# Performance work log

Hardware: AMD Instinct MI355X
Metric: run time of the kernel (lower is better)

The kernel has to match this reference:

```python
import jax, jax.numpy as jnp
import numpy as np

N, E = 50000, 800000
IN_DIM, HID, ZDIM = 256, 128, 64
LN_EPS = 1e-5


def _layernorm(x, gamma, beta):
    mu = jnp.mean(x, axis=-1, keepdims=True)
    var = jnp.mean(jnp.square(x - mu), axis=-1, keepdims=True)
    return (x - mu) * jax.lax.rsqrt(var + LN_EPS) * gamma + beta


def _gcn_conv(h, src, dst, dinv, W, b):
    # h: (N, d_in) -> (N, d_out). GCNConv: X W, then sym-normalized
    # aggregation over edges with self-loops, then bias.
    h = h @ W                                   # (N, d_out)
    coef = dinv[src] * dinv[dst]                # (E,)
    agg = jax.ops.segment_sum(h[src] * coef[:, None], dst,
                              num_segments=h.shape[0])
    agg = agg + h * jnp.square(dinv)[:, None]   # self-loop term
    return agg + b


def setup_inputs() -> dict:
    key = jax.random.key(0)
    ks = jax.random.split(key, 5)
    x = jax.random.normal(ks[0], (N, IN_DIM), dtype=jnp.float32)
    edge_index = jax.random.randint(ks[1], (2, E), 0, N, dtype=jnp.int64)
    s1 = 1.0 / np.sqrt(IN_DIM)
    s2 = 1.0 / np.sqrt(HID)
    return {
        "x": x,
        "edge_index": edge_index,
        "ln_gamma": jnp.ones((IN_DIM,), jnp.float32),
        "ln_beta": jnp.zeros((IN_DIM,), jnp.float32),
        "W1": jax.random.normal(ks[2], (IN_DIM, HID), jnp.float32) * s1,
        "b1": jnp.zeros((HID,), jnp.float32),
        "W2": jax.random.normal(ks[3], (HID, HID), jnp.float32) * s2,
        "b2": jnp.zeros((HID,), jnp.float32),
        "W3": jax.random.normal(ks[4], (HID, ZDIM), jnp.float32) * s2,
        "b3": jnp.zeros((ZDIM,), jnp.float32),
    }


def reference(x, edge_index, ln_gamma, ln_beta, W1, b1, W2, b2, W3, b3):
    src, dst = edge_index[0], edge_index[1]
    n = x.shape[0]
    # degree with self-loops (dropout is inference no-op, training=False)
    deg = jnp.ones((n,), x.dtype).at[dst].add(1.0)
    dinv = jax.lax.rsqrt(deg)
    h = _layernorm(x, ln_gamma, ln_beta)
    h = jax.nn.relu(_gcn_conv(h, src, dst, dinv, W1, b1))
    h = jax.nn.relu(_gcn_conv(h, src, dst, dinv, W2, b2))
    z = _gcn_conv(h, src, dst, dinv, W3, b3)
    return z
```

## Files before the change

### kernel.cpp

```cpp
#include <hip/hip_runtime.h>
#include <cstdint>
#include <cstddef>


typedef __attribute__((ext_vector_type(8))) __bf16 bf16x8;
typedef __attribute__((ext_vector_type(4))) float f32x4;
typedef _Float16 half_t;
typedef __attribute__((ext_vector_type(8))) _Float16 half8_t;

#define NHIST 256
#define CHUNK 4096
#define MAXB 8192

__global__ __launch_bounds__(256) void prep_misc(
    const int* __restrict__ dst,
    const float* __restrict__ W1, const float* __restrict__ W2,
    const float* __restrict__ W3,
    int* __restrict__ bcnt_multi,
    unsigned short* __restrict__ W1t_hi, unsigned short* __restrict__ W1t_lo,
    unsigned short* __restrict__ W2t_hi, unsigned short* __restrict__ W2t_lo,
    unsigned short* __restrict__ W3t_hi, unsigned short* __restrict__ W3t_lo,
    int E) {
  int blk = blockIdx.x;
  int tid = threadIdx.x;
  if (blk < NHIST) {
    __shared__ int h[256];
    h[tid] = 0;
    __syncthreads();
    for (int e = blk * 256 + tid; e < E; e += NHIST * 256)
      atomicAdd(&h[dst[e] >> 8], 1);
    __syncthreads();
    bcnt_multi[blk * 256 + tid] = h[tid];
    return;
  }
  int idx = (blk - NHIST) * 256 + tid;
  if (idx < 32768) {
    int k = idx / 128, c = idx % 128;
    float v = W1[idx];
    __bf16 h = (__bf16)v;
    __bf16 l = (__bf16)(v - (float)h);
    W1t_hi[(size_t)c * 256 + k] = __builtin_bit_cast(unsigned short, h);
    W1t_lo[(size_t)c * 256 + k] = __builtin_bit_cast(unsigned short, l);
    return;
  }
  const float* W;
  unsigned short *Th, *Tl;
  int K, NOUT;
  if (idx < 49152) {
    idx -= 32768;
    W = W2; Th = W2t_hi; Tl = W2t_lo; K = 128; NOUT = 128;
  } else {
    idx -= 49152;
    W = W3; Th = W3t_hi; Tl = W3t_lo; K = 128; NOUT = 64;
  }
  int k = idx / NOUT, c = idx % NOUT;
  float v = W[idx];
  half_t h = (half_t)v;
  half_t l = (half_t)((v - (float)h) * 2048.0f);
  Th[(size_t)c * K + k] = __builtin_bit_cast(unsigned short, h);
  Tl[(size_t)c * K + k] = __builtin_bit_cast(unsigned short, l);
}

__global__ __launch_bounds__(256) void scan_buckets(const int* __restrict__ bcnt_multi,
                                                    int* __restrict__ bbase,
                                                    int* __restrict__ bcur, int NB, int E) {
  __shared__ int tmp[256];
  int t = threadIdx.x;
  int v = 0;
  for (int h = 0; h < NHIST; ++h) v += bcnt_multi[h * 256 + t];
  tmp[t] = v;
  __syncthreads();
  for (int off = 1; off < 256; off <<= 1) {
    int x = (t >= off) ? tmp[t - off] : 0;
    __syncthreads();
    tmp[t] += x;
    __syncthreads();
  }
  int excl = tmp[t] - v;
  if (t < NB) { bbase[t] = excl; bcur[t] = excl; }
  if (t == 0) bbase[NB] = E;
}

__device__ __forceinline__ void scatter_body(char* smem_raw, int bid,
                                             const int* __restrict__ src,
                                             const int* __restrict__ dst,
                                             int* __restrict__ bcur,
                                             unsigned int* __restrict__ binned, int E) {
  unsigned int* recs = (unsigned int*)smem_raw;
  int* hist = (int*)(smem_raw + 16384);
  int* lbase = hist + 256;
  int* resv = lbase + 256;
  int* cur = resv + 256;
  int t = threadIdx.x;
  int e0 = bid * CHUNK;
  if (e0 >= E) return;
  int len = min(CHUNK, E - e0);
  hist[t] = 0;
  cur[t] = 0;
  __syncthreads();
  for (int i = t; i < len; i += 256) atomicAdd(&hist[dst[e0 + i] >> 8], 1);
  __syncthreads();
  int v = hist[t];
  lbase[t] = v;
  __syncthreads();
  for (int off = 1; off < 256; off <<= 1) {
    int x = (t >= off) ? lbase[t - off] : 0;
    __syncthreads();
    lbase[t] += x;
    __syncthreads();
  }
  int myexcl = lbase[t] - v;
  if (v) resv[t] = atomicAdd(&bcur[t], v);
  __syncthreads();
  lbase[t] = myexcl;
  __syncthreads();
  for (int i = t; i < len; i += 256) {
    int d = dst[e0 + i], s = src[e0 + i];
    int b = d >> 8;
    int r = atomicAdd(&cur[b], 1);
    recs[lbase[b] + r] = ((unsigned int)d << 16) | (unsigned int)s;
  }
  __syncthreads();
  for (int i = t; i < len; i += 256) {
    unsigned int rc = recs[i];
    int b = rc >> 24;
    binned[resv[b] + (i - lbase[b])] = rc;
  }
}

__device__ __forceinline__ void sort_body(char* smem_raw, int b,
                                          const unsigned int* __restrict__ binned,
                                          const int* __restrict__ bbase,
                                          int* __restrict__ srcs,
                                          int* __restrict__ offs,
                                          float* __restrict__ dinv,
                                          int N, int NB, int E) {
  int* sstage = (int*)smem_raw;
  int* hist = (int*)(smem_raw + 32768);
  int* nbase = hist + 256;
  int* cur = nbase + 256;
  int* tmp = cur + 256;
  int t = threadIdx.x;
  int base = bbase[b], end = bbase[b + 1];
  int L = end - base;
  if (L > MAXB) L = MAXB;
  hist[t] = 0;
  __syncthreads();
  for (int i = t; i < L; i += 256)
    atomicAdd(&hist[(binned[base + i] >> 16) & 255], 1);
  __syncthreads();
  int v = hist[t];
  tmp[t] = v;
  __syncthreads();
  for (int off = 1; off < 256; off <<= 1) {
    int x = (t >= off) ? tmp[t - off] : 0;
    __syncthreads();
    tmp[t] += x;
    __syncthreads();
  }
  int excl = tmp[t] - v;
  nbase[t] = excl;
  cur[t] = excl;
  int node = (b << 8) + t;
  if (node < N) {
    offs[node] = base + excl;
    dinv[node] = rsqrtf(1.0f + (float)v);
  }
  if (b == NB - 1 && t == 0) offs[N] = E;
  __syncthreads();
  for (int i = t; i < L; i += 256) {
    unsigned int p = binned[base + i];
    int ld = (p >> 16) & 255;
    int slot = atomicAdd(&cur[ld], 1);
    sstage[slot] = (int)(p & 0xFFFFu);
  }
  __syncthreads();
  for (int i = t; i < L; i += 256) srcs[base + i] = sstage[i];
}

template <int K, int NOUT, bool LN, bool A_FP16>
__device__ __forceinline__ void gemm_body(char* smem_raw, int gbid,
                                          const void* __restrict__ Avoid,
                                          const unsigned short* __restrict__ Wt_hi,
                                          const unsigned short* __restrict__ Wt_lo,
                                          const float* __restrict__ gamma,
                                          const float* __restrict__ beta,
                                          half_t* __restrict__ out, int nrows) {
  constexpr int BM = 32, BK = 32, BKP = BK + 8;
  constexpr int NTW = NOUT / 32;

  const int tid = threadIdx.x;
  const int lane = tid & 63;
  const int w = tid >> 6;
  const int quad = lane >> 4;
  const int l16 = lane & 15;
  const int rg = (w & 1) * 16;
  const int cg = (w >> 1) * (NOUT / 2);
  const int row0 = gbid * BM;

  if constexpr (!A_FP16) {
    unsigned short* As_hi = (unsigned short*)smem_raw;
    unsigned short* As_lo = As_hi + BM * BKP;
    unsigned short* Bs_hi = As_lo + BM * BKP;
    unsigned short* Bs_lo = Bs_hi + NOUT * BKP;
    float* mu_s = (float*)(Bs_lo + NOUT * BKP);
    float* rs_s = mu_s + BM;
    const float* A = (const float*)Avoid;

    if constexpr (LN) {
      int r = tid >> 3;
      int part = tid & 7;
      int grow = row0 + r;
      if (grow > nrows - 1) grow = nrows - 1;
      const float4* rp = (const float4*)(A + (size_t)grow * K);
      float s = 0.f, s2 = 0.f;
#pragma unroll
      for (int j = 0; j < K / 32; ++j) {
        float4 v = rp[part * (K / 32) + j];
        s += v.x + v.y + v.z + v.w;
        s2 += v.x * v.x + v.y * v.y + v.z * v.z + v.w * v.w;
      }
      s += __shfl_xor(s, 1);
      s += __shfl_xor(s, 2);
      s += __shfl_xor(s, 4);
      s2 += __shfl_xor(s2, 1);
      s2 += __shfl_xor(s2, 2);
      s2 += __shfl_xor(s2, 4);
      if (part == 0) {
        float m = s * (1.0f / (float)K);
        float var = s2 * (1.0f / (float)K) - m * m;
        mu_s[r] = m;
        rs_s[r] = rsqrtf(var + 1e-5f);
      }
      __syncthreads();
    }

    f32x4 acc[NTW];
#pragma unroll
    for (int t = 0; t < NTW; ++t) acc[t] = (f32x4){0.f, 0.f, 0.f, 0.f};

    for (int k0 = 0; k0 < K; k0 += BK) {
      {
        int r = tid >> 3;
        int c4 = (tid & 7) * 4;
        int grow = row0 + r;
        if (grow > nrows - 1) grow = nrows - 1;
        float4 v = *(const float4*)&A[(size_t)grow * K + k0 + c4];
        if constexpr (LN) {
          float m = mu_s[r], s = rs_s[r];
          float4 g = *(const float4*)&gamma[k0 + c4];
          float4 b = *(const float4*)&beta[k0 + c4];
          v.x = (v.x - m) * s * g.x + b.x;
          v.y = (v.y - m) * s * g.y + b.y;
          v.z = (v.z - m) * s * g.z + b.z;
          v.w = (v.w - m) * s * g.w + b.w;
        }
        float vv[4] = {v.x, v.y, v.z, v.w};
#pragma unroll
        for (int j = 0; j < 4; ++j) {
          __bf16 h = (__bf16)vv[j];
          __bf16 l = (__bf16)(vv[j] - (float)h);
          As_hi[r * BKP + c4 + j] = __builtin_bit_cast(unsigned short, h);
          As_lo[r * BKP + c4 + j] = __builtin_bit_cast(unsigned short, l);
        }
      }
#pragma unroll
      for (int i = 0; i < NOUT / 64; ++i) {
        int n = i * 64 + (tid >> 2);
        int c8 = (tid & 3) * 8;
        *(uint4*)&Bs_hi[n * BKP + c8] = *(const uint4*)&Wt_hi[(size_t)n * K + k0 + c8];
        *(uint4*)&Bs_lo[n * BKP + c8] = *(const uint4*)&Wt_lo[(size_t)n * K + k0 + c8];
      }
      __syncthreads();

      bf16x8 ah = *(const bf16x8*)&As_hi[(rg + l16) * BKP + quad * 8];
      bf16x8 al = *(const bf16x8*)&As_lo[(rg + l16) * BKP + quad * 8];
#pragma unroll
      for (int t = 0; t < NTW; ++t) {
        bf16x8 bh = *(const bf16x8*)&Bs_hi[(cg + t * 16 + l16) * BKP + quad * 8];
        bf16x8 bl = *(const bf16x8*)&Bs_lo[(cg + t * 16 + l16) * BKP + quad * 8];
        acc[t] = __builtin_amdgcn_mfma_f32_16x16x32_bf16(ah, bh, acc[t], 0, 0, 0);
        acc[t] = __builtin_amdgcn_mfma_f32_16x16x32_bf16(al, bh, acc[t], 0, 0, 0);
        acc[t] = __builtin_amdgcn_mfma_f32_16x16x32_bf16(ah, bl, acc[t], 0, 0, 0);
      }
      __syncthreads();
    }

#pragma unroll
    for (int t = 0; t < NTW; ++t) {
#pragma unroll
      for (int r = 0; r < 4; ++r) {
        int grow = row0 + rg + quad * 4 + r;
        if (grow < nrows)
          out[(size_t)grow * NOUT + cg + t * 16 + l16] = (half_t)acc[t][r];
      }
    }
  } else {
    half_t* As = (half_t*)smem_raw;
    half_t* Bs_hi = As + BM * BKP;
    half_t* Bs_lo = Bs_hi + NOUT * BKP;
    const half_t* A = (const half_t*)Avoid;

    f32x4 acc1[NTW], acc2[NTW];
#pragma unroll
    for (int t = 0; t < NTW; ++t) {
      acc1[t] = (f32x4){0.f, 0.f, 0.f, 0.f};
      acc2[t] = (f32x4){0.f, 0.f, 0.f, 0.f};
    }

    for (int k0 = 0; k0 < K; k0 += BK) {
      {
        int r = tid >> 3;
        int c4 = (tid & 7) * 4;
        int grow = row0 + r;
        if (grow > nrows - 1) grow = nrows - 1;
        *(uint2*)&As[r * BKP + c4] = *(const uint2*)&A[(size_t)grow * K + k0 + c4];
      }
#pragma unroll
      for (int i = 0; i < NOUT / 64; ++i) {
        int n = i * 64 + (tid >> 2);
        int c8 = (tid & 3) * 8;
        *(uint4*)&Bs_hi[n * BKP + c8] =
            *(const uint4*)&Wt_hi[(size_t)n * K + k0 + c8];
        *(uint4*)&Bs_lo[n * BKP + c8] =
            *(const uint4*)&Wt_lo[(size_t)n * K + k0 + c8];
      }
      __syncthreads();

      half8_t av = *(const half8_t*)&As[(rg + l16) * BKP + quad * 8];
#pragma unroll
      for (int t = 0; t < NTW; ++t) {
        half8_t bh = *(const half8_t*)&Bs_hi[(cg + t * 16 + l16) * BKP + quad * 8];
        half8_t bl = *(const half8_t*)&Bs_lo[(cg + t * 16 + l16) * BKP + quad * 8];
        acc1[t] = __builtin_amdgcn_mfma_f32_16x16x32_f16(av, bh, acc1[t], 0, 0, 0);
        acc2[t] = __builtin_amdgcn_mfma_f32_16x16x32_f16(av, bl, acc2[t], 0, 0, 0);
      }
      __syncthreads();
    }

#pragma unroll
    for (int t = 0; t < NTW; ++t) {
#pragma unroll
      for (int r = 0; r < 4; ++r) {
        int grow = row0 + rg + quad * 4 + r;
        if (grow < nrows)
          out[(size_t)grow * NOUT + cg + t * 16 + l16] =
              (half_t)(acc1[t][r] + acc2[t][r] * (1.0f / 2048.0f));
      }
    }
  }
}

constexpr int GEMM1_SMEM = 32 * 40 * 4 + 128 * 40 * 4 + 256;
__global__ __launch_bounds__(256) void fused_scatter_gemm1(
    const int* __restrict__ src, const int* __restrict__ dst,
    int* __restrict__ bcur, unsigned int* __restrict__ binned, int E,
    const float* __restrict__ x,
    const unsigned short* __restrict__ W1t_hi, const unsigned short* __restrict__ W1t_lo,
    const float* __restrict__ gamma, const float* __restrict__ beta,
    half_t* __restrict__ t, int nrows, int nscat) {
  __shared__ __align__(16) char smem[GEMM1_SMEM];
  if ((int)blockIdx.x < nscat)
    scatter_body(smem, blockIdx.x, src, dst, bcur, binned, E);
  else
    gemm_body<256, 128, true, false>(smem, blockIdx.x - nscat, x, W1t_hi, W1t_lo,
                                     gamma, beta, t, nrows);
}

__global__ __launch_bounds__(256) void fused_sort_gemm1(
    const unsigned int* __restrict__ binned, const int* __restrict__ bbase,
    int* __restrict__ srcs, int* __restrict__ offs, float* __restrict__ dinv,
    int N, int NB, int E,
    const float* __restrict__ x,
    const unsigned short* __restrict__ W1t_hi, const unsigned short* __restrict__ W1t_lo,
    const float* __restrict__ gamma, const float* __restrict__ beta,
    half_t* __restrict__ t, int nrows, int g1a) {
  __shared__ __align__(16) char smem[36864];
  if ((int)blockIdx.x < NB)
    sort_body(smem, blockIdx.x, binned, bbase, srcs, offs, dinv, N, NB, E);
  else
    gemm_body<256, 128, true, false>(smem, g1a + (blockIdx.x - NB), x, W1t_hi, W1t_lo,
                                     gamma, beta, t, nrows);
}

template <int K, int NOUT>
__launch_bounds__(256)
__global__ void gemm_k(const half_t* __restrict__ A,
                       const unsigned short* __restrict__ Wt_hi,
                       const unsigned short* __restrict__ Wt_lo,
                       half_t* __restrict__ out, int nrows) {
  constexpr int SM = 32 * 40 * 2 + NOUT * 40 * 4;
  __shared__ __align__(16) char smem[SM];
  gemm_body<K, NOUT, false, true>(smem, blockIdx.x, A, Wt_hi, Wt_lo,
                                  nullptr, nullptr, out, nrows);
}

__global__ __launch_bounds__(256) void agg128_h(const half_t* __restrict__ t,
                                                const int* __restrict__ offs,
                                                const int* __restrict__ srcs,
                                                const float* __restrict__ dinv,
                                                const float* __restrict__ bias,
                                                half_t* __restrict__ out, int n) {
  int gid = blockIdx.x * blockDim.x + threadIdx.x;
  int node = gid >> 6, lane = gid & 63;
  if (node >= n) return;
  int qw = lane >> 4;
  int fl = lane & 15;
  int e0 = offs[node], e1 = offs[node + 1];
  float acc[8] = {0.f, 0.f, 0.f, 0.f, 0.f, 0.f, 0.f, 0.f};
  int e = e0 + qw;
  for (; e + 12 < e1; e += 16) {
    int sa = srcs[e], sb = srcs[e + 4], sc = srcs[e + 8], sd = srcs[e + 12];
    float wa = dinv[sa], wb = dinv[sb], wc = dinv[sc], wd = dinv[sd];
    half8_t va = *(const half8_t*)(t + ((size_t)sa << 7) + fl * 8);
    half8_t vb = *(const half8_t*)(t + ((size_t)sb << 7) + fl * 8);
    half8_t vc = *(const half8_t*)(t + ((size_t)sc << 7) + fl * 8);
    half8_t vd = *(const half8_t*)(t + ((size_t)sd << 7) + fl * 8);
#pragma unroll
    for (int j = 0; j < 8; ++j) {
      acc[j] = fmaf(wa, (float)va[j], acc[j]);
      acc[j] = fmaf(wb, (float)vb[j], acc[j]);
      acc[j] = fmaf(wc, (float)vc[j], acc[j]);
      acc[j] = fmaf(wd, (float)vd[j], acc[j]);
    }
  }
  for (; e < e1; e += 4) {
    int s = srcs[e];
    float w = dinv[s];
    half8_t v = *(const half8_t*)(t + ((size_t)s << 7) + fl * 8);
#pragma unroll
    for (int j = 0; j < 8; ++j) acc[j] = fmaf(w, (float)v[j], acc[j]);
  }
#pragma unroll
  for (int j = 0; j < 8; ++j) {
    acc[j] += __shfl_xor(acc[j], 16);
    acc[j] += __shfl_xor(acc[j], 32);
  }
  if (qw == 0) {
    float di = dinv[node];
    float dii = di * di;
    half8_t sv = *(const half8_t*)(t + ((size_t)node << 7) + fl * 8);
    float4 b0 = *(const float4*)(bias + fl * 8);
    float4 b1 = *(const float4*)(bias + fl * 8 + 4);
    float bb[8] = {b0.x, b0.y, b0.z, b0.w, b1.x, b1.y, b1.z, b1.w};
    half8_t o;
#pragma unroll
    for (int j = 0; j < 8; ++j) {
      float v = di * acc[j] + dii * (float)sv[j] + bb[j];
      o[j] = (half_t)fmaxf(v, 0.f);
    }
    *(half8_t*)(out + ((size_t)node << 7) + fl * 8) = o;
  }
}

__global__ __launch_bounds__(256) void agg64_h(const half_t* __restrict__ t,
                                               const int* __restrict__ offs,
                                               const int* __restrict__ srcs,
                                               const float* __restrict__ dinv,
                                               const float* __restrict__ bias,
                                               float* __restrict__ out, int n) {
  int gid = blockIdx.x * blockDim.x + threadIdx.x;
  int node = gid >> 6, lane = gid & 63;
  if (node >= n) return;
  int og = lane >> 3;
  int fl = lane & 7;
  int e0 = offs[node], e1 = offs[node + 1];
  float acc[8] = {0.f, 0.f, 0.f, 0.f, 0.f, 0.f, 0.f, 0.f};
  int e = e0 + og;
  for (; e + 8 < e1; e += 16) {
    int sa = srcs[e], sb = srcs[e + 8];
    float wa = dinv[sa], wb = dinv[sb];
    half8_t va = *(const half8_t*)(t + ((size_t)sa << 6) + fl * 8);
    half8_t vb = *(const half8_t*)(t + ((size_t)sb << 6) + fl * 8);
#pragma unroll
    for (int j = 0; j < 8; ++j) {
      acc[j] = fmaf(wa, (float)va[j], acc[j]);
      acc[j] = fmaf(wb, (float)vb[j], acc[j]);
    }
  }
  for (; e < e1; e += 8) {
    int s = srcs[e];
    float w = dinv[s];
    half8_t v = *(const half8_t*)(t + ((size_t)s << 6) + fl * 8);
#pragma unroll
    for (int j = 0; j < 8; ++j) acc[j] = fmaf(w, (float)v[j], acc[j]);
  }
#pragma unroll
  for (int j = 0; j < 8; ++j) {
    acc[j] += __shfl_xor(acc[j], 8);
    acc[j] += __shfl_xor(acc[j], 16);
    acc[j] += __shfl_xor(acc[j], 32);
  }
  if (og == 0) {
    float di = dinv[node];
    float dii = di * di;
    half8_t sv = *(const half8_t*)(t + ((size_t)node << 6) + fl * 8);
    float4 b0 = *(const float4*)(bias + fl * 8);
    float4 b1 = *(const float4*)(bias + fl * 8 + 4);
    float bb[8] = {b0.x, b0.y, b0.z, b0.w, b1.x, b1.y, b1.z, b1.w};
    float ov[8];
#pragma unroll
    for (int j = 0; j < 8; ++j) ov[j] = di * acc[j] + dii * (float)sv[j] + bb[j];
    *(float4*)(out + ((size_t)node << 6) + fl * 8) = make_float4(ov[0], ov[1], ov[2], ov[3]);
    *(float4*)(out + ((size_t)node << 6) + fl * 8 + 4) = make_float4(ov[4], ov[5], ov[6], ov[7]);
  }
}

extern "C" void kernel_launch(void* const* d_in, const int* in_sizes, int n_in,
                              void* d_out, int out_size, void* d_ws, size_t ws_size,
                              hipStream_t stream) {
  const float* x = (const float*)d_in[0];
  const int* ei = (const int*)d_in[1];
  const float* gamma = (const float*)d_in[2];
  const float* beta = (const float*)d_in[3];
  const float* W1 = (const float*)d_in[4];
  const float* b1 = (const float*)d_in[5];
  const float* W2 = (const float*)d_in[6];
  const float* b2 = (const float*)d_in[7];
  const float* W3 = (const float*)d_in[8];
  const float* b3 = (const float*)d_in[9];
  float* out = (float*)d_out;

  const int N = in_sizes[0] / 256;
  const int E = in_sizes[1] / 2;
  const int* src = ei;
  const int* dst = ei + E;
  const int NB = (N + 255) >> 8;

  char* ws = (char*)d_ws;
  auto alloc = [&](size_t bytes) -> char* {
    char* p = ws;
    ws += (bytes + 255) & ~(size_t)255;
    return p;
  };
  int* bcnt_multi = (int*)alloc(NHIST * 256 * 4);
  int* bbase = (int*)alloc(257 * 4);
  int* bcur = (int*)alloc(256 * 4);
  unsigned int* binned = (unsigned int*)alloc((size_t)E * 4);
  int* srcs = (int*)alloc((size_t)E * 4);
  int* offs = (int*)alloc((size_t)(N + 1) * 4);
  float* dinv = (float*)alloc((size_t)N * 4);
  half_t* t = (half_t*)alloc((size_t)N * 128 * 2);
  half_t* h = (half_t*)alloc((size_t)N * 128 * 2);
  unsigned short* W1t_hi = (unsigned short*)alloc(256 * 128 * 2);
  unsigned short* W1t_lo = (unsigned short*)alloc(256 * 128 * 2);
  unsigned short* W2t_hi = (unsigned short*)alloc(128 * 128 * 2);
  unsigned short* W2t_lo = (unsigned short*)alloc(128 * 128 * 2);
  unsigned short* W3t_hi = (unsigned short*)alloc(128 * 64 * 2);
  unsigned short* W3t_lo = (unsigned short*)alloc(128 * 64 * 2);

  prep_misc<<<NHIST + 224, 256, 0, stream>>>(
      dst, W1, W2, W3, bcnt_multi, W1t_hi, W1t_lo, W2t_hi, W2t_lo,
      W3t_hi, W3t_lo, E);

  scan_buckets<<<1, 256, 0, stream>>>(bcnt_multi, bbase, bcur, NB, E);

  const int gemm_blocks = (N + 31) / 32;
  const int G1A = gemm_blocks / 2;
  const int G1B = gemm_blocks - G1A;
  const int NSCAT = (E + CHUNK - 1) / CHUNK;
  const int agg_blocks = (N + 3) / 4;

  fused_scatter_gemm1<<<NSCAT + G1A, 256, 0, stream>>>(
      src, dst, bcur, binned, E, x, W1t_hi, W1t_lo, gamma, beta, t, N, NSCAT);

  fused_sort_gemm1<<<NB + G1B, 256, 0, stream>>>(
      binned, bbase, srcs, offs, dinv, N, NB, E, x, W1t_hi, W1t_lo, gamma, beta,
      t, N, G1A);

  agg128_h<<<agg_blocks, 256, 0, stream>>>(t, offs, srcs, dinv, b1, h, N);

  gemm_k<128, 128><<<gemm_blocks, 256, 0, stream>>>(h, W2t_hi, W2t_lo, t, N);
  agg128_h<<<agg_blocks, 256, 0, stream>>>(t, offs, srcs, dinv, b2, h, N);

  gemm_k<128, 64><<<gemm_blocks, 256, 0, stream>>>(h, W3t_hi, W3t_lo, t, N);
  agg64_h<<<agg_blocks, 256, 0, stream>>>(t, offs, srcs, dinv, b3, out, N);
}
```

Baseline: 268.7 us.

## Fuse edge aggregation with the following layer GEMM in one kernel

Replaces the separate agg128_h and gemm_k launches for layers 1-2 and 2-3 with a single agg_gemm kernel. Each block aggregates 32 destination rows into shared memory as fp16, then multiplies that tile by the next weight matrix with MFMA. This removes one launch per layer and the global write and reread of the aggregated hidden activations. In exchange, each node is now gathered by 16 threads with no edge-parallel split, so there is less memory-level parallelism per node, and the blocks are larger, which may lower occupancy.

```diff
diff --git a/kernel.cpp b/kernel.cpp
--- a/kernel.cpp
+++ b/kernel.cpp
@@ -178,9 +178,9 @@
   for (int i = t; i < L; i += 256) srcs[base + i] = sstage[i];
 }
 
-template <int K, int NOUT, bool LN, bool A_FP16>
+template <int K, int NOUT, bool LN>
 __device__ __forceinline__ void gemm_body(char* smem_raw, int gbid,
-                                          const void* __restrict__ Avoid,
+                                          const float* __restrict__ A,
                                           const unsigned short* __restrict__ Wt_hi,
                                           const unsigned short* __restrict__ Wt_lo,
                                           const float* __restrict__ gamma,
@@ -198,160 +198,105 @@
   const int cg = (w >> 1) * (NOUT / 2);
   const int row0 = gbid * BM;
 
-  if constexpr (!A_FP16) {
-    unsigned short* As_hi = (unsigned short*)smem_raw;
-    unsigned short* As_lo = As_hi + BM * BKP;
-    unsigned short* Bs_hi = As_lo + BM * BKP;
-    unsigned short* Bs_lo = Bs_hi + NOUT * BKP;
-    float* mu_s = (float*)(Bs_lo + NOUT * BKP);
-    float* rs_s = mu_s + BM;
-    const float* A = (const float*)Avoid;
-
-    if constexpr (LN) {
+  unsigned short* As_hi = (unsigned short*)smem_raw;
+  unsigned short* As_lo = As_hi + BM * BKP;
+  unsigned short* Bs_hi = As_lo + BM * BKP;
+  unsigned short* Bs_lo = Bs_hi + NOUT * BKP;
+  float* mu_s = (float*)(Bs_lo + NOUT * BKP);
+  float* rs_s = mu_s + BM;
+
+  if constexpr (LN) {
+    int r = tid >> 3;
+    int part = tid & 7;
+    int grow = row0 + r;
+    if (grow > nrows - 1) grow = nrows - 1;
+    const float4* rp = (const float4*)(A + (size_t)grow * K);
+    float s = 0.f, s2 = 0.f;
+#pragma unroll
+    for (int j = 0; j < K / 32; ++j) {
+      float4 v = rp[part * (K / 32) + j];
+      s += v.x + v.y + v.z + v.w;
+      s2 += v.x * v.x + v.y * v.y + v.z * v.z + v.w * v.w;
+    }
+    s += __shfl_xor(s, 1);
+    s += __shfl_xor(s, 2);
+    s += __shfl_xor(s, 4);
+    s2 += __shfl_xor(s2, 1);
+    s2 += __shfl_xor(s2, 2);
+    s2 += __shfl_xor(s2, 4);
+    if (part == 0) {
+      float m = s * (1.0f / (float)K);
+      float var = s2 * (1.0f / (float)K) - m * m;
+      mu_s[r] = m;
+      rs_s[r] = rsqrtf(var + 1e-5f);
+    }
+    __syncthreads();
+  }
+
+  f32x4 acc[NTW];
+#pragma unroll
+  for (int t = 0; t < NTW; ++t) acc[t] = (f32x4){0.f, 0.f, 0.f, 0.f};
+
+  for (int k0 = 0; k0 < K; k0 += BK) {
+    {
       int r = tid >> 3;
-      int part = tid & 7;
+      int c4 = (tid & 7) * 4;
       int grow = row0 + r;
       if (grow > nrows - 1) grow = nrows - 1;
-      const float4* rp = (const float4*)(A + (size_t)grow * K);
-      float s = 0.f, s2 = 0.f;
-#pragma unroll
-      for (int j = 0; j < K / 32; ++j) {
-        float4 v = rp[part * (K / 32) + j];
-        s += v.x + v.y + v.z + v.w;
-        s2 += v.x * v.x + v.y * v.y + v.z * v.z + v.w * v.w;
+      float4 v = *(const float4*)&A[(size_t)grow * K + k0 + c4];
+      if constexpr (LN) {
+        float m = mu_s[r], s = rs_s[r];
+        float4 g = *(const float4*)&gamma[k0 + c4];
+        float4 b = *(const float4*)&beta[k0 + c4];
+        v.x = (v.x - m) * s * g.x + b.x;
+        v.y = (v.y - m) * s * g.y + b.y;
+        v.z = (v.z - m) * s * g.z + b.z;
+        v.w = (v.w - m) * s * g.w + b.w;
       }
-      s += __shfl_xor(s, 1);
-      s += __shfl_xor(s, 2);
-      s += __shfl_xor(s, 4);
-      s2 += __shfl_xor(s2, 1);
-      s2 += __shfl_xor(s2, 2);
-      s2 += __shfl_xor(s2, 4);
-      if (part == 0) {
-        float m = s * (1.0f / (float)K);
-        float var = s2 * (1.0f / (float)K) - m * m;
-        mu_s[r] = m;
-        rs_s[r] = rsqrtf(var + 1e-5f);
+      float vv[4] = {v.x, v.y, v.z, v.w};
+#pragma unroll
+      for (int j = 0; j < 4; ++j) {
+        __bf16 h = (__bf16)vv[j];
+        __bf16 l = (__bf16)(vv[j] - (float)h);
+        As_hi[r * BKP + c4 + j] = __builtin_bit_cast(unsigned short, h);
+        As_lo[r * BKP + c4 + j] = __builtin_bit_cast(unsigned short, l);
       }
-      __syncthreads();
-    }
-
-    f32x4 acc[NTW];
-#pragma unroll
-    for (int t = 0; t < NTW; ++t) acc[t] = (f32x4){0.f, 0.f, 0.f, 0.f};
-
-    for (int k0 = 0; k0 < K; k0 += BK) {
-      {
-        int r = tid >> 3;
-        int c4 = (tid & 7) * 4;
-        int grow = row0 + r;
-        if (grow > nrows - 1) grow = nrows - 1;
-        float4 v = *(const float4*)&A[(size_t)grow * K + k0 + c4];
-        if constexpr (LN) {
-          float m = mu_s[r], s = rs_s[r];
-          float4 g = *(const float4*)&gamma[k0 + c4];
-          float4 b = *(const float4*)&beta[k0 + c4];
-          v.x = (v.x - m) * s * g.x + b.x;
-          v.y = (v.y - m) * s * g.y + b.y;
-          v.z = (v.z - m) * s * g.z + b.z;
-          v.w = (v.w - m) * s * g.w + b.w;
-        }
-        float vv[4] = {v.x, v.y, v.z, v.w};
-#pragma unroll
-        for (int j = 0; j < 4; ++j) {
-          __bf16 h = (__bf16)vv[j];
-          __bf16 l = (__bf16)(vv[j] - (float)h);
-          As_hi[r * BKP + c4 + j] = __builtin_bit_cast(unsigned short, h);
-          As_lo[r * BKP + c4 + j] = __builtin_bit_cast(unsigned short, l);
-        }
-      }
-#pragma unroll
-      for (int i = 0; i < NOUT / 64; ++i) {
-        int n = i * 64 + (tid >> 2);
-        int c8 = (tid & 3) * 8;
-        *(uint4*)&Bs_hi[n * BKP + c8] = *(const uint4*)&Wt_hi[(size_t)n * K + k0 + c8];
-        *(uint4*)&Bs_lo[n * BKP + c8] = *(const uint4*)&Wt_lo[(size_t)n * K + k0 + c8];
-      }
-      __syncthreads();
-
-      bf16x8 ah = *(const bf16x8*)&As_hi[(rg + l16) * BKP + quad * 8];
-      bf16x8 al = *(const bf16x8*)&As_lo[(rg + l16) * BKP + quad * 8];
-#pragma unroll
-      for (int t = 0; t < NTW; ++t) {
-        bf16x8 bh = *(const bf16x8*)&Bs_hi[(cg + t * 16 + l16) * BKP + quad * 8];
-        bf16x8 bl = *(const bf16x8*)&Bs_lo[(cg + t * 16 + l16) * BKP + quad * 8];
-        acc[t] = __builtin_amdgcn_mfma_f32_16x16x32_bf16(ah, bh, acc[t], 0, 0, 0);
-        acc[t] = __builtin_amdgcn_mfma_f32_16x16x32_bf16(al, bh, acc[t], 0, 0, 0);
-        acc[t] = __builtin_amdgcn_mfma_f32_16x16x32_bf16(ah, bl, acc[t], 0, 0, 0);
-      }
-      __syncthreads();
-    }
-
+    }
+#pragma unroll
+    for (int i = 0; i < NOUT / 64; ++i) {
+      int n = i * 64 + (tid >> 2);
+      int c8 = (tid & 3) * 8;
+      *(uint4*)&Bs_hi[n * BKP + c8] = *(const uint4*)&Wt_hi[(size_t)n * K + k0 + c8];
+      *(uint4*)&Bs_lo[n * BKP + c8] = *(const uint4*)&Wt_lo[(size_t)n * K + k0 + c8];
+    }
+    __syncthreads();
+
+    bf16x8 ah = *(const bf16x8*)&As_hi[(rg + l16) * BKP + quad * 8];
+    bf16x8 al = *(const bf16x8*)&As_lo[(rg + l16) * BKP + quad * 8];
 #pragma unroll
     for (int t = 0; t < NTW; ++t) {
-#pragma unroll
-      for (int r = 0; r < 4; ++r) {
-        int grow = row0 + rg + quad * 4 + r;
-        if (grow < nrows)
-          out[(size_t)grow * NOUT + cg + t * 16 + l16] = (half_t)acc[t][r];
-      }
-    }
-  } else {
-    half_t* As = (half_t*)smem_raw;
-    half_t* Bs_hi = As + BM * BKP;
-    half_t* Bs_lo = Bs_hi + NOUT * BKP;
-    const half_t* A = (const half_t*)Avoid;
-
-    f32x4 acc1[NTW], acc2[NTW];
-#pragma unroll
-    for (int t = 0; t < NTW; ++t) {
-      acc1[t] = (f32x4){0.f, 0.f, 0.f, 0.f};
-      acc2[t] = (f32x4){0.f, 0.f, 0.f, 0.f};
-    }
-
-    for (int k0 = 0; k0 < K; k0 += BK) {
-      {
-        int r = tid >> 3;
-        int c4 = (tid & 7) * 4;
-        int grow = row0 + r;
-        if (grow > nrows - 1) grow = nrows - 1;
-        *(uint2*)&As[r * BKP + c4] = *(const uint2*)&A[(size_t)grow * K + k0 + c4];
-      }
-#pragma unroll
-      for (int i = 0; i < NOUT / 64; ++i) {
-        int n = i * 64 + (tid >> 2);
-        int c8 = (tid & 3) * 8;
-        *(uint4*)&Bs_hi[n * BKP + c8] =
-            *(const uint4*)&Wt_hi[(size_t)n * K + k0 + c8];
-        *(uint4*)&Bs_lo[n * BKP + c8] =
-            *(const uint4*)&Wt_lo[(size_t)n * K + k0 + c8];
-      }
-      __syncthreads();
-
-      half8_t av = *(const half8_t*)&As[(rg + l16) * BKP + quad * 8];
-#pragma unroll
-      for (int t = 0; t < NTW; ++t) {
-        half8_t bh = *(const half8_t*)&Bs_hi[(cg + t * 16 + l16) * BKP + quad * 8];
-        half8_t bl = *(const half8_t*)&Bs_lo[(cg + t * 16 + l16) * BKP + quad * 8];
-        acc1[t] = __builtin_amdgcn_mfma_f32_16x16x32_f16(av, bh, acc1[t], 0, 0, 0);
-        acc2[t] = __builtin_amdgcn_mfma_f32_16x16x32_f16(av, bl, acc2[t], 0, 0, 0);
-      }
-      __syncthreads();
-    }
-
-#pragma unroll
-    for (int t = 0; t < NTW; ++t) {
-#pragma unroll
-      for (int r = 0; r < 4; ++r) {
-        int grow = row0 + rg + quad * 4 + r;
-        if (grow < nrows)
-          out[(size_t)grow * NOUT + cg + t * 16 + l16] =
-              (half_t)(acc1[t][r] + acc2[t][r] * (1.0f / 2048.0f));
-      }
+      bf16x8 bh = *(const bf16x8*)&Bs_hi[(cg + t * 16 + l16) * BKP + quad * 8];
+      bf16x8 bl = *(const bf16x8*)&Bs_lo[(cg + t * 16 + l16) * BKP + quad * 8];
+      acc[t] = __builtin_amdgcn_mfma_f32_16x16x32_bf16(ah, bh, acc[t], 0, 0, 0);
+      acc[t] = __builtin_amdgcn_mfma_f32_16x16x32_bf16(al, bh, acc[t], 0, 0, 0);
+      acc[t] = __builtin_amdgcn_mfma_f32_16x16x32_bf16(ah, bl, acc[t], 0, 0, 0);
+    }
+    __syncthreads();
+  }
+
+#pragma unroll
+  for (int t = 0; t < NTW; ++t) {
+#pragma unroll
+    for (int r = 0; r < 4; ++r) {
+      int grow = row0 + rg + quad * 4 + r;
+      if (grow < nrows)
+        out[(size_t)grow * NOUT + cg + t * 16 + l16] = (half_t)acc[t][r];
     }
   }
 }
 
 constexpr int GEMM1_SMEM = 32 * 40 * 4 + 128 * 40 * 4 + 256;
+
 __global__ __launch_bounds__(256) void fused_scatter_gemm1(
     const int* __restrict__ src, const int* __restrict__ dst,
     int* __restrict__ bcur, unsigned int* __restrict__ binned, int E,
@@ -363,8 +308,8 @@
   if ((int)blockIdx.x < nscat)
     scatter_body(smem, blockIdx.x, src, dst, bcur, binned, E);
   else
-    gemm_body<256, 128, true, false>(smem, blockIdx.x - nscat, x, W1t_hi, W1t_lo,
-                                     gamma, beta, t, nrows);
+    gemm_body<256, 128, true>(smem, blockIdx.x - nscat, x, W1t_hi, W1t_lo,
+                              gamma, beta, t, nrows);
 }
 
 __global__ __launch_bounds__(256) void fused_sort_gemm1(
@@ -379,77 +324,117 @@
   if ((int)blockIdx.x < NB)
     sort_body(smem, blockIdx.x, binned, bbase, srcs, offs, dinv, N, NB, E);
   else
-    gemm_body<256, 128, true, false>(smem, g1a + (blockIdx.x - NB), x, W1t_hi, W1t_lo,
-                                     gamma, beta, t, nrows);
-}
-
-template <int K, int NOUT>
-__launch_bounds__(256)
-__global__ void gemm_k(const half_t* __restrict__ A,
-                       const unsigned short* __restrict__ Wt_hi,
-                       const unsigned short* __restrict__ Wt_lo,
-                       half_t* __restrict__ out, int nrows) {
-  constexpr int SM = 32 * 40 * 2 + NOUT * 40 * 4;
-  __shared__ __align__(16) char smem[SM];
-  gemm_body<K, NOUT, false, true>(smem, blockIdx.x, A, Wt_hi, Wt_lo,
-                                  nullptr, nullptr, out, nrows);
-}
-
-__global__ __launch_bounds__(256) void agg128_h(const half_t* __restrict__ t,
-                                                const int* __restrict__ offs,
-                                                const int* __restrict__ srcs,
-                                                const float* __restrict__ dinv,
-                                                const float* __restrict__ bias,
-                                                half_t* __restrict__ out, int n) {
-  int gid = blockIdx.x * blockDim.x + threadIdx.x;
-  int node = gid >> 6, lane = gid & 63;
-  if (node >= n) return;
-  int qw = lane >> 4;
-  int fl = lane & 15;
-  int e0 = offs[node], e1 = offs[node + 1];
-  float acc[8] = {0.f, 0.f, 0.f, 0.f, 0.f, 0.f, 0.f, 0.f};
-  int e = e0 + qw;
-  for (; e + 12 < e1; e += 16) {
-    int sa = srcs[e], sb = srcs[e + 4], sc = srcs[e + 8], sd = srcs[e + 12];
-    float wa = dinv[sa], wb = dinv[sb], wc = dinv[sc], wd = dinv[sd];
-    half8_t va = *(const half8_t*)(t + ((size_t)sa << 7) + fl * 8);
-    half8_t vb = *(const half8_t*)(t + ((size_t)sb << 7) + fl * 8);
-    half8_t vc = *(const half8_t*)(t + ((size_t)sc << 7) + fl * 8);
-    half8_t vd = *(const half8_t*)(t + ((size_t)sd << 7) + fl * 8);
-#pragma unroll
-    for (int j = 0; j < 8; ++j) {
-      acc[j] = fmaf(wa, (float)va[j], acc[j]);
-      acc[j] = fmaf(wb, (float)vb[j], acc[j]);
-      acc[j] = fmaf(wc, (float)vc[j], acc[j]);
-      acc[j] = fmaf(wd, (float)vd[j], acc[j]);
-    }
-  }
-  for (; e < e1; e += 4) {
-    int s = srcs[e];
-    float w = dinv[s];
-    half8_t v = *(const half8_t*)(t + ((size_t)s << 7) + fl * 8);
-#pragma unroll
-    for (int j = 0; j < 8; ++j) acc[j] = fmaf(w, (float)v[j], acc[j]);
-  }
-#pragma unroll
-  for (int j = 0; j < 8; ++j) {
-    acc[j] += __shfl_xor(acc[j], 16);
-    acc[j] += __shfl_xor(acc[j], 32);
-  }
-  if (qw == 0) {
-    float di = dinv[node];
-    float dii = di * di;
-    half8_t sv = *(const half8_t*)(t + ((size_t)node << 7) + fl * 8);
-    float4 b0 = *(const float4*)(bias + fl * 8);
-    float4 b1 = *(const float4*)(bias + fl * 8 + 4);
-    float bb[8] = {b0.x, b0.y, b0.z, b0.w, b1.x, b1.y, b1.z, b1.w};
-    half8_t o;
-#pragma unroll
-    for (int j = 0; j < 8; ++j) {
-      float v = di * acc[j] + dii * (float)sv[j] + bb[j];
-      o[j] = (half_t)fmaxf(v, 0.f);
-    }
-    *(half8_t*)(out + ((size_t)node << 7) + fl * 8) = o;
+    gemm_body<256, 128, true>(smem, g1a + (blockIdx.x - NB), x, W1t_hi, W1t_lo,
+                              gamma, beta, t, nrows);
+}
+
+template <int NOUT>
+__global__ __launch_bounds__(256) void agg_gemm(
+    const half_t* __restrict__ tin,
+    const int* __restrict__ offs, const int* __restrict__ srcs,
+    const float* __restrict__ dinv, const float* __restrict__ bias,
+    const unsigned short* __restrict__ Wt_hi,
+    const unsigned short* __restrict__ Wt_lo,
+    half_t* __restrict__ out, int nrows) {
+  constexpr int K = 128, BK = 32, BKP = BK + 8, ROWP = K + 8;
+  constexpr int NTW = NOUT / 32;
+  __shared__ __align__(16) half_t As[32 * ROWP];
+  __shared__ __align__(16) half_t Bs_hi[NOUT * BKP];
+  __shared__ __align__(16) half_t Bs_lo[NOUT * BKP];
+
+  const int tid = threadIdx.x;
+  const int row0 = blockIdx.x * 32;
+
+  {
+    int g = tid >> 4, fl = tid & 15;
+#pragma unroll
+    for (int rr = g; rr < 32; rr += 16) {
+      int node = row0 + rr;
+      if (node > nrows - 1) node = nrows - 1;
+      int e0 = offs[node], e1 = offs[node + 1];
+      float acc[8] = {0.f, 0.f, 0.f, 0.f, 0.f, 0.f, 0.f, 0.f};
+      int e = e0;
+      for (; e + 3 < e1; e += 4) {
+        int sa = srcs[e], sb = srcs[e + 1], sc = srcs[e + 2], sd = srcs[e + 3];
+        float wa = dinv[sa], wb = dinv[sb], wc = dinv[sc], wd = dinv[sd];
+        half8_t va = *(const half8_t*)(tin + ((size_t)sa << 7) + fl * 8);
+        half8_t vb = *(const half8_t*)(tin + ((size_t)sb << 7) + fl * 8);
+        half8_t vc = *(const half8_t*)(tin + ((size_t)sc << 7) + fl * 8);
+        half8_t vd = *(const half8_t*)(tin + ((size_t)sd << 7) + fl * 8);
+#pragma unroll
+        for (int j = 0; j < 8; ++j) {
+          acc[j] = fmaf(wa, (float)va[j], acc[j]);
+          acc[j] = fmaf(wb, (float)vb[j], acc[j]);
+          acc[j] = fmaf(wc, (float)vc[j], acc[j]);
+          acc[j] = fmaf(wd, (float)vd[j], acc[j]);
+        }
+      }
+      for (; e < e1; ++e) {
+        int s = srcs[e];
+        float w = dinv[s];
+        half8_t v = *(const half8_t*)(tin + ((size_t)s << 7) + fl * 8);
+#pragma unroll
+        for (int j = 0; j < 8; ++j) acc[j] = fmaf(w, (float)v[j], acc[j]);
+      }
+      float di = dinv[node];
+      float dii = di * di;
+      half8_t sv = *(const half8_t*)(tin + ((size_t)node << 7) + fl * 8);
+      float4 b0 = *(const float4*)(bias + fl * 8);
+      float4 b1 = *(const float4*)(bias + fl * 8 + 4);
+      float bb[8] = {b0.x, b0.y, b0.z, b0.w, b1.x, b1.y, b1.z, b1.w};
+#pragma unroll
+      for (int j = 0; j < 8; ++j) {
+        float v = di * acc[j] + dii * (float)sv[j] + bb[j];
+        As[rr * ROWP + fl * 8 + j] = (half_t)fmaxf(v, 0.f);
+      }
+    }
+  }
+  __syncthreads();
+
+  const int lane = tid & 63;
+  const int w = tid >> 6;
+  const int quad = lane >> 4;
+  const int l16 = lane & 15;
+  const int rg = (w & 1) * 16;
+  const int cg = (w >> 1) * (NOUT / 2);
+
+  f32x4 acc1[NTW], acc2[NTW];
+#pragma unroll
+  for (int t = 0; t < NTW; ++t) {
+    acc1[t] = (f32x4){0.f, 0.f, 0.f, 0.f};
+    acc2[t] = (f32x4){0.f, 0.f, 0.f, 0.f};
+  }
+
+  for (int k0 = 0; k0 < K; k0 += BK) {
+#pragma unroll
+    for (int i = 0; i < NOUT / 64; ++i) {
+      int n = i * 64 + (tid >> 2);
+      int c8 = (tid & 3) * 8;
+      *(uint4*)&Bs_hi[n * BKP + c8] = *(const uint4*)&Wt_hi[(size_t)n * K + k0 + c8];
+      *(uint4*)&Bs_lo[n * BKP + c8] = *(const uint4*)&Wt_lo[(size_t)n * K + k0 + c8];
+    }
+    __syncthreads();
+
+    half8_t av = *(const half8_t*)&As[(rg + l16) * ROWP + k0 + quad * 8];
+#pragma unroll
+    for (int t = 0; t < NTW; ++t) {
+      half8_t bh = *(const half8_t*)&Bs_hi[(cg + t * 16 + l16) * BKP + quad * 8];
+      half8_t bl = *(const half8_t*)&Bs_lo[(cg + t * 16 + l16) * BKP + quad * 8];
+      acc1[t] = __builtin_amdgcn_mfma_f32_16x16x32_f16(av, bh, acc1[t], 0, 0, 0);
+      acc2[t] = __builtin_amdgcn_mfma_f32_16x16x32_f16(av, bl, acc2[t], 0, 0, 0);
+    }
+    __syncthreads();
+  }
+
+#pragma unroll
+  for (int t = 0; t < NTW; ++t) {
+#pragma unroll
+    for (int r = 0; r < 4; ++r) {
+      int grow = row0 + rg + quad * 4 + r;
+      if (grow < nrows)
+        out[(size_t)grow * NOUT + cg + t * 16 + l16] =
+            (half_t)(acc1[t][r] + acc2[t][r] * (1.0f / 2048.0f));
+    }
   }
 }
 
@@ -568,11 +553,11 @@
       binned, bbase, srcs, offs, dinv, N, NB, E, x, W1t_hi, W1t_lo, gamma, beta,
       t, N, G1A);
 
-  agg128_h<<<agg_blocks, 256, 0, stream>>>(t, offs, srcs, dinv, b1, h, N);
-
-  gemm_k<128, 128><<<gemm_blocks, 256, 0, stream>>>(h, W2t_hi, W2t_lo, t, N);
-  agg128_h<<<agg_blocks, 256, 0, stream>>>(t, offs, srcs, dinv, b2, h, N);
-
-  gemm_k<128, 64><<<gemm_blocks, 256, 0, stream>>>(h, W3t_hi, W3t_lo, t, N);
+  agg_gemm<128><<<gemm_blocks, 256, 0, stream>>>(
+      t, offs, srcs, dinv, b1, W2t_hi, W2t_lo, h, N);
+
+  agg_gemm<64><<<gemm_blocks, 256, 0, stream>>>(
+      h, offs, srcs, dinv, b2, W3t_hi, W3t_lo, t, N);
+
   agg64_h<<<agg_blocks, 256, 0, stream>>>(t, offs, srcs, dinv, b3, out, N);
 }
```

After: 258.7 us, median of 3. 3.7% less time.
